# Kernel tuning notes

Hardware: AMD Instinct MI355X
Metric: run time of the kernel (lower is better)

The kernel has to match this reference:

```python
import jax, jax.numpy as jnp
import numpy as np

BS, N, C = 16, 128, 512
EPS = 1e-5


def setup_inputs() -> dict:
    key = jax.random.key(0)
    ks = jax.random.split(key, 6)
    x = jax.random.normal(ks[0], (BS, N, C), dtype=jnp.float32)
    y = jax.random.normal(ks[1], (BS, C), dtype=jnp.float32)
    # edge conv: Conv2d(2C -> 1, 1x1), init std sqrt(2/(1*1*1))
    conv_e_w = jax.random.normal(ks[2], (1, 2 * C), dtype=jnp.float32) * np.sqrt(2.0)
    conv_e_b = jnp.zeros((1,), dtype=jnp.float32)
    bn_e_g = jnp.ones((1,), dtype=jnp.float32)
    bn_e_b = jnp.zeros((1,), dtype=jnp.float32)
    bn_e_m = jnp.zeros((1,), dtype=jnp.float32)
    bn_e_v = jnp.ones((1,), dtype=jnp.float32)
    # feature conv: Conv2d(2C -> C, 1x1), init std sqrt(2/C)
    conv_f_w = jax.random.normal(ks[3], (C, 2 * C), dtype=jnp.float32) * np.sqrt(2.0 / C)
    conv_f_b = jnp.zeros((C,), dtype=jnp.float32)
    bn_f_g = jnp.ones((C,), dtype=jnp.float32)
    bn_f_b = jnp.zeros((C,), dtype=jnp.float32)
    bn_f_m = jnp.zeros((C,), dtype=jnp.float32)
    bn_f_v = jnp.ones((C,), dtype=jnp.float32)
    return {
        "x": x, "y": y,
        "conv_e_w": conv_e_w, "conv_e_b": conv_e_b,
        "bn_e_g": bn_e_g, "bn_e_b": bn_e_b, "bn_e_m": bn_e_m, "bn_e_v": bn_e_v,
        "conv_f_w": conv_f_w, "conv_f_b": conv_f_b,
        "bn_f_g": bn_f_g, "bn_f_b": bn_f_b, "bn_f_m": bn_f_m, "bn_f_v": bn_f_v,
    }


def reference(x, y, conv_e_w, conv_e_b, bn_e_g, bn_e_b, bn_e_m, bn_e_v,
              conv_f_w, conv_f_b, bn_f_g, bn_f_b, bn_f_m, bn_f_v):
    bs, n, c = x.shape
    # ---- Wcompute: pairwise |x_i - x_j| -> conv1x1(2C->1) + BN + mask + softmax ----
    diff = jnp.abs(x[:, :, None, :] - x[:, None, :, :])  # [bs, N, N, C]
    w_diff = conv_e_w[0, :c]   # weights on pairwise-diff channels
    w_y = conv_e_w[0, c:]      # weights on broadcast y channels
    # 1x1 conv collapses to einsum; y part is constant over (i, j)
    score = (jnp.einsum('bijc,c->bij', diff, w_diff)
             + (y @ w_y)[:, None, None] + conv_e_b[0])  # [bs, N, N]
    # BatchNorm2d(1), inference mode
    score = (score - bn_e_m[0]) * (bn_e_g[0] * jax.lax.rsqrt(bn_e_v[0] + EPS)) + bn_e_b[0]
    # mask diagonal (W_id * 1e8) then softmax over neighbors j
    score = score - jnp.eye(n, dtype=score.dtype)[None] * 1e8
    W = jax.nn.softmax(score, axis=2)  # [bs, N, N]
    # ---- Gconv: neighbor aggregation + conv1x1(2C->C) + BN + ReLU ----
    x_nb = jnp.einsum('bij,bjc->bic', W, x)       # [bs, N, C]
    h = jnp.concatenate([x, x_nb], axis=2)        # [bs, N, 2C]
    out = jnp.einsum('bnk,ck->bnc', h, conv_f_w) + conv_f_b  # [bs, N, C]
    # BatchNorm2d(C), inference mode (per-channel)
    out = (out - bn_f_m) * (bn_f_g * jax.lax.rsqrt(bn_f_v + EPS)) + bn_f_b
    return jax.nn.relu(out)
```

## Files before the change

kernel.cpp:

```cpp
#include <hip/hip_runtime.h>
#include <hip/hip_bf16.h>

#define NTOK 128
#define CHN  512
#define KTOT 1024
#define EPSV 1e-5f

typedef __attribute__((ext_vector_type(8))) short bf16x8;
typedef __attribute__((ext_vector_type(4))) float f32x4;

union BfPack4 { ushort4 u; __hip_bfloat16 h[4]; };


__global__ __launch_bounds__(256)
void k0_transpose(const float* __restrict__ xg,
                  float* __restrict__ xT,
                  __hip_bfloat16* __restrict__ xTbf,
                  __hip_bfloat16* __restrict__ hb,
                  const float* __restrict__ wf,
                  __hip_bfloat16* __restrict__ wfb)
{
    __shared__ float ts[64 * 68];
    const int t  = threadIdx.x;
    const int bk = blockIdx.x;
    const int b  = bk >> 4;
    const int jt = (bk >> 3) & 1;
    const int ct = bk & 7;
    const int j0 = jt * 64, c0 = ct * 64;

    const int jr = t >> 2, qd = t & 3;
    const float* src = xg + ((size_t)(b * NTOK) + j0 + jr) * CHN + c0 + qd * 16;
    float4 v0 = *(const float4*)&src[0];
    float4 v1 = *(const float4*)&src[4];
    float4 v2 = *(const float4*)&src[8];
    float4 v3 = *(const float4*)&src[12];
    *(float4*)&ts[jr * 68 + qd * 16 + 0]  = v0;
    *(float4*)&ts[jr * 68 + qd * 16 + 4]  = v1;
    *(float4*)&ts[jr * 68 + qd * 16 + 8]  = v2;
    *(float4*)&ts[jr * 68 + qd * 16 + 12] = v3;

    {
        __hip_bfloat16* hrow = hb + ((size_t)(b * NTOK) + j0 + jr) * KTOT + c0 + qd * 16;
        BfPack4 p;
        p.h[0]=__float2bfloat16(v0.x); p.h[1]=__float2bfloat16(v0.y);
        p.h[2]=__float2bfloat16(v0.z); p.h[3]=__float2bfloat16(v0.w);
        *(ushort4*)&hrow[0] = p.u;
        p.h[0]=__float2bfloat16(v1.x); p.h[1]=__float2bfloat16(v1.y);
        p.h[2]=__float2bfloat16(v1.z); p.h[3]=__float2bfloat16(v1.w);
        *(ushort4*)&hrow[4] = p.u;
        p.h[0]=__float2bfloat16(v2.x); p.h[1]=__float2bfloat16(v2.y);
        p.h[2]=__float2bfloat16(v2.z); p.h[3]=__float2bfloat16(v2.w);
        *(ushort4*)&hrow[8] = p.u;
        p.h[0]=__float2bfloat16(v3.x); p.h[1]=__float2bfloat16(v3.y);
        p.h[2]=__float2bfloat16(v3.z); p.h[3]=__float2bfloat16(v3.w);
        *(ushort4*)&hrow[12] = p.u;
    }

    {
        const int r   = 2 * bk + (t >> 7);
        const int col = (t & 127) * 8;
        const float* wsrc = wf + (size_t)r * KTOT + col;
        float4 u0 = *(const float4*)&wsrc[0];
        float4 u1 = *(const float4*)&wsrc[4];
        BfPack4 p;
        p.h[0]=__float2bfloat16(u0.x); p.h[1]=__float2bfloat16(u0.y);
        p.h[2]=__float2bfloat16(u0.z); p.h[3]=__float2bfloat16(u0.w);
        *(ushort4*)&wfb[(size_t)r * KTOT + col] = p.u;
        p.h[0]=__float2bfloat16(u1.x); p.h[1]=__float2bfloat16(u1.y);
        p.h[2]=__float2bfloat16(u1.z); p.h[3]=__float2bfloat16(u1.w);
        *(ushort4*)&wfb[(size_t)r * KTOT + col + 4] = p.u;
    }
    __syncthreads();

    const int cs = t >> 4, jj = (t & 15) * 4;
    #pragma unroll
    for (int m = 0; m < 4; ++m) {
        const int c = cs + 16 * m;
        float4 o;
        o.x = ts[(jj + 0) * 68 + c];
        o.y = ts[(jj + 1) * 68 + c];
        o.z = ts[(jj + 2) * 68 + c];
        o.w = ts[(jj + 3) * 68 + c];
        const size_t base = ((size_t)(b * CHN) + c0 + c) * NTOK + j0 + jj;
        *(float4*)&xT[base] = o;
        BfPack4 p;
        p.h[0]=__float2bfloat16(o.x); p.h[1]=__float2bfloat16(o.y);
        p.h[2]=__float2bfloat16(o.z); p.h[3]=__float2bfloat16(o.w);
        *(ushort4*)&xTbf[base] = p.u;
    }
}

__global__ __launch_bounds__(512)
void k1_fused(const float* __restrict__ xg,
              const float* __restrict__ xT,
              const float* __restrict__ wde,
              const float* __restrict__ bn_e_g,
              const float* __restrict__ bn_e_v,
              const __hip_bfloat16* __restrict__ xTbf,
              __hip_bfloat16* __restrict__ hb)
{
    __shared__ float        pLDS[4][8][128];
    __shared__ __hip_bfloat16 Wlds[16][136];

    const int t  = threadIdx.x;
    const int w  = t >> 6;
    const int l  = t & 63;
    const int bk = blockIdx.x;
    const int b  = bk >> 4;
    const int i0 = (bk & 15) * 8;

    {
        const int rp = __builtin_amdgcn_readfirstlane(w >> 2);
        const int cq = __builtin_amdgcn_readfirstlane(w & 3);
        const int c0 = cq * 128;
        const int r0 = rp * 4;

        const float* __restrict__ xtp = xT + ((size_t)(b * CHN) + c0) * NTOK + l;
        const float* __restrict__ xip = xg + ((size_t)(b * NTOK) + i0 + r0) * CHN + c0;
        const float* __restrict__ wdp = wde + c0;

        float a00=0.f,a01=0.f,a10=0.f,a11=0.f,a20=0.f,a21=0.f,a30=0.f,a31=0.f;
        #pragma unroll 8
        for (int c = 0; c < 128; ++c) {
            const float xj1 = xtp[c * NTOK];
            const float xj2 = xtp[c * NTOK + 64];
            const float wd  = wdp[c];
            const float xi0 = xip[0 * CHN + c];
            const float xi1 = xip[1 * CHN + c];
            const float xi2 = xip[2 * CHN + c];
            const float xi3 = xip[3 * CHN + c];
            a00 += fabsf(xi0 - xj1) * wd;  a01 += fabsf(xi0 - xj2) * wd;
            a10 += fabsf(xi1 - xj1) * wd;  a11 += fabsf(xi1 - xj2) * wd;
            a20 += fabsf(xi2 - xj1) * wd;  a21 += fabsf(xi2 - xj2) * wd;
            a30 += fabsf(xi3 - xj1) * wd;  a31 += fabsf(xi3 - xj2) * wd;
        }
        pLDS[cq][r0 + 0][l] = a00;  pLDS[cq][r0 + 0][l + 64] = a01;
        pLDS[cq][r0 + 1][l] = a10;  pLDS[cq][r0 + 1][l + 64] = a11;
        pLDS[cq][r0 + 2][l] = a20;  pLDS[cq][r0 + 2][l + 64] = a21;
        pLDS[cq][r0 + 3][l] = a30;  pLDS[cq][r0 + 3][l + 64] = a31;
    }
    __syncthreads();

    {
        float p1 = pLDS[0][w][l]      + pLDS[1][w][l]
                 + pLDS[2][w][l]      + pLDS[3][w][l];
        float p2 = pLDS[0][w][l + 64] + pLDS[1][w][l + 64]
                 + pLDS[2][w][l + 64] + pLDS[3][w][l + 64];
        const float sc = bn_e_g[0] * rsqrtf(bn_e_v[0] + EPSV);
        const int ir = i0 + w;
        float l1 = p1 * sc - (l == ir ? 1e8f : 0.f);
        float l2 = p2 * sc - (l + 64 == ir ? 1e8f : 0.f);

        float m = fmaxf(l1, l2);
        #pragma unroll
        for (int off = 32; off > 0; off >>= 1) m = fmaxf(m, __shfl_xor(m, off));
        const float e1 = __expf(l1 - m);
        const float e2 = __expf(l2 - m);
        float ssum = e1 + e2;
        #pragma unroll
        for (int off = 32; off > 0; off >>= 1) ssum += __shfl_xor(ssum, off);
        const float inv = 1.f / ssum;

        Wlds[w][l]          = __float2bfloat16(e1 * inv);
        Wlds[w][l + 64]     = __float2bfloat16(e2 * inv);
        Wlds[w + 8][l]      = __float2bfloat16(0.f);
        Wlds[w + 8][l + 64] = __float2bfloat16(0.f);
    }
    __syncthreads();

    {
        const int m16 = l & 15;
        const int q   = l >> 4;

        bf16x8 afr[4];
        #pragma unroll
        for (int kk = 0; kk < 4; ++kk)
            afr[kk] = *(const bf16x8*)&Wlds[m16][q * 8 + kk * 32];

        const int cbase = w * 64;
        #pragma unroll
        for (int ni = 0; ni < 4; ++ni) {
            const int c = cbase + ni * 16 + m16;
            const short* B0 = (const short*)xTbf + ((size_t)(b * CHN) + c) * NTOK + q * 8;
            f32x4 acc = {0.f, 0.f, 0.f, 0.f};
            #pragma unroll
            for (int kk = 0; kk < 4; ++kk) {
                const bf16x8 bfr = *(const bf16x8*)(B0 + kk * 32);
                acc = __builtin_amdgcn_mfma_f32_16x16x32_bf16(afr[kk], bfr, acc, 0, 0, 0);
            }
            if (q < 2) {
                #pragma unroll
                for (int r = 0; r < 4; ++r) {
                    const int i = i0 + q * 4 + r;
                    hb[(size_t)(b * NTOK + i) * KTOT + CHN + c] = __float2bfloat16(acc[r]);
                }
            }
        }
    }
}

__global__ __launch_bounds__(256)
void k2_gemm_bn_relu(const __hip_bfloat16* __restrict__ hbp,
                     const __hip_bfloat16* __restrict__ wfbp,
                     const float* __restrict__ fb,
                     const float* __restrict__ gg,
                     const float* __restrict__ bb,
                     const float* __restrict__ mm,
                     const float* __restrict__ vv,
                     float* __restrict__ out)
{
    const int blk  = blockIdx.x;
    const int r0   = (blk >> 3) << 6;
    const int c0   = (blk & 7) << 6;
    const int t    = threadIdx.x;
    const int w    = t >> 6;
    const int lane = t & 63;
    const int wm   = w & 1;
    const int wn   = w >> 1;
    const int m16  = lane & 15;
    const int qq   = lane >> 4;

    const short* A0 = (const short*)hbp  + (size_t)(r0 + wm * 32 + m16) * KTOT + qq * 8;
    const short* B0 = (const short*)wfbp + (size_t)(c0 + wn * 32 + m16) * KTOT + qq * 8;

    f32x4 acc00 = {0.f, 0.f, 0.f, 0.f};
    f32x4 acc01 = acc00, acc10 = acc00, acc11 = acc00;

    #pragma unroll 4
    for (int k0 = 0; k0 < KTOT; k0 += 32) {
        const bf16x8 aA = *(const bf16x8*)(A0 + k0);
        const bf16x8 aB = *(const bf16x8*)(A0 + 16 * KTOT + k0);
        const bf16x8 bA = *(const bf16x8*)(B0 + k0);
        const bf16x8 bB = *(const bf16x8*)(B0 + 16 * KTOT + k0);
        acc00 = __builtin_amdgcn_mfma_f32_16x16x32_bf16(aA, bA, acc00, 0, 0, 0);
        acc01 = __builtin_amdgcn_mfma_f32_16x16x32_bf16(aA, bB, acc01, 0, 0, 0);
        acc10 = __builtin_amdgcn_mfma_f32_16x16x32_bf16(aB, bA, acc10, 0, 0, 0);
        acc11 = __builtin_amdgcn_mfma_f32_16x16x32_bf16(aB, bB, acc11, 0, 0, 0);
    }

    #pragma unroll
    for (int ni = 0; ni < 2; ++ni) {
        const int c = c0 + wn * 32 + ni * 16 + m16;
        const float gf = gg[c] * rsqrtf(vv[c] + EPSV);
        const float ad = fb[c] - mm[c];
        const float bv = bb[c];
        const f32x4 acr0 = ni ? acc01 : acc00;
        const f32x4 acr1 = ni ? acc11 : acc10;
        #pragma unroll
        for (int r2 = 0; r2 < 4; ++r2) {
            int row = r0 + wm * 32 + qq * 4 + r2;
            float val = (acr0[r2] + ad) * gf + bv;
            out[(size_t)row * CHN + c] = fmaxf(val, 0.f);
            row += 16;
            val = (acr1[r2] + ad) * gf + bv;
            out[(size_t)row * CHN + c] = fmaxf(val, 0.f);
        }
    }
}

extern "C" void kernel_launch(void* const* d_in, const int* in_sizes, int n_in,
                              void* d_out, int out_size, void* d_ws, size_t ws_size,
                              hipStream_t stream) {
    const float* x        = (const float*)d_in[0];
    const float* conv_e_w = (const float*)d_in[2];
    const float* bn_e_g   = (const float*)d_in[4];
    const float* bn_e_v   = (const float*)d_in[7];
    const float* conv_f_w = (const float*)d_in[8];
    const float* conv_f_b = (const float*)d_in[9];
    const float* bn_f_g   = (const float*)d_in[10];
    const float* bn_f_b   = (const float*)d_in[11];
    const float* bn_f_m   = (const float*)d_in[12];
    const float* bn_f_v   = (const float*)d_in[13];
    float* out = (float*)d_out;

    char* ws = (char*)d_ws;
    float*           xT   = (float*)(ws);
    __hip_bfloat16*  hb   = (__hip_bfloat16*)(ws + (12u << 20));
    __hip_bfloat16*  wfb  = (__hip_bfloat16*)(ws + (16u << 20));
    __hip_bfloat16*  xTbf = (__hip_bfloat16*)(ws + (17u << 20) + (512u << 10));

    k0_transpose<<<256, 256, 0, stream>>>(x, xT, xTbf, hb, conv_f_w, wfb);
    k1_fused<<<256, 512, 0, stream>>>(x, xT, conv_e_w, bn_e_g, bn_e_v, xTbf, hb);
    k2_gemm_bn_relu<<<256, 256, 0, stream>>>(hb, wfb, conv_f_b, bn_f_g, bn_f_b,
                                             bn_f_m, bn_f_v, out);
}
```

Before: 120.4 us.

## Merge three kernels into one cooperative kernel with grid-wide syncs

Replaces the transpose, fused softmax/aggregation, and GEMM kernels with a single cooperative kernel of 256 blocks by 512 threads, separated by grid.sync barriers. This removes two kernel launch gaps and the drain between them. The pairwise-distance loop is also rewritten to process two channels at a time with float2 vectors and max(d,-d) for the absolute value. The trade-offs are grid-barrier cost, half the threads sitting idle in the GEMM phase, and higher LDS and register use limiting occupancy.

```diff
diff --git a/kernel.cpp b/kernel.cpp
--- a/kernel.cpp
+++ b/kernel.cpp
@@ -1,5 +1,8 @@
 #include <hip/hip_runtime.h>
 #include <hip/hip_bf16.h>
+#include <hip/hip_cooperative_groups.h>
+
+namespace cg = cooperative_groups;
 
 #define NTOK 128
 #define CHN  512
@@ -8,252 +11,241 @@
 
 typedef __attribute__((ext_vector_type(8))) short bf16x8;
 typedef __attribute__((ext_vector_type(4))) float f32x4;
+typedef __attribute__((ext_vector_type(2))) float f32x2;
 
 union BfPack4 { ushort4 u; __hip_bfloat16 h[4]; };
 
 
-__global__ __launch_bounds__(256)
-void k0_transpose(const float* __restrict__ xg,
-                  float* __restrict__ xT,
-                  __hip_bfloat16* __restrict__ xTbf,
-                  __hip_bfloat16* __restrict__ hb,
-                  const float* __restrict__ wf,
-                  __hip_bfloat16* __restrict__ wfb)
+__global__ __launch_bounds__(512)
+void mega(const float* __restrict__ xg,
+          float* __restrict__ xT,
+          __hip_bfloat16* __restrict__ xTbf,
+          __hip_bfloat16* __restrict__ hb,
+          const float* __restrict__ wf,
+          __hip_bfloat16* __restrict__ wfb,
+          const float* __restrict__ wde,
+          const float* __restrict__ bn_e_g,
+          const float* __restrict__ bn_e_v,
+          const float* __restrict__ fb,
+          const float* __restrict__ gg,
+          const float* __restrict__ bb,
+          const float* __restrict__ mm,
+          const float* __restrict__ vv,
+          float* __restrict__ out)
 {
-    __shared__ float ts[64 * 68];
-    const int t  = threadIdx.x;
-    const int bk = blockIdx.x;
-    const int b  = bk >> 4;
-    const int jt = (bk >> 3) & 1;
-    const int ct = bk & 7;
-    const int j0 = jt * 64, c0 = ct * 64;
-
-    const int jr = t >> 2, qd = t & 3;
-    const float* src = xg + ((size_t)(b * NTOK) + j0 + jr) * CHN + c0 + qd * 16;
-    float4 v0 = *(const float4*)&src[0];
-    float4 v1 = *(const float4*)&src[4];
-    float4 v2 = *(const float4*)&src[8];
-    float4 v3 = *(const float4*)&src[12];
-    *(float4*)&ts[jr * 68 + qd * 16 + 0]  = v0;
-    *(float4*)&ts[jr * 68 + qd * 16 + 4]  = v1;
-    *(float4*)&ts[jr * 68 + qd * 16 + 8]  = v2;
-    *(float4*)&ts[jr * 68 + qd * 16 + 12] = v3;
-
-    {
-        __hip_bfloat16* hrow = hb + ((size_t)(b * NTOK) + j0 + jr) * KTOT + c0 + qd * 16;
-        BfPack4 p;
-        p.h[0]=__float2bfloat16(v0.x); p.h[1]=__float2bfloat16(v0.y);
-        p.h[2]=__float2bfloat16(v0.z); p.h[3]=__float2bfloat16(v0.w);
-        *(ushort4*)&hrow[0] = p.u;
-        p.h[0]=__float2bfloat16(v1.x); p.h[1]=__float2bfloat16(v1.y);
-        p.h[2]=__float2bfloat16(v1.z); p.h[3]=__float2bfloat16(v1.w);
-        *(ushort4*)&hrow[4] = p.u;
-        p.h[0]=__float2bfloat16(v2.x); p.h[1]=__float2bfloat16(v2.y);
-        p.h[2]=__float2bfloat16(v2.z); p.h[3]=__float2bfloat16(v2.w);
-        *(ushort4*)&hrow[8] = p.u;
-        p.h[0]=__float2bfloat16(v3.x); p.h[1]=__float2bfloat16(v3.y);
-        p.h[2]=__float2bfloat16(v3.z); p.h[3]=__float2bfloat16(v3.w);
-        *(ushort4*)&hrow[12] = p.u;
-    }
-
-    {
-        const int r   = 2 * bk + (t >> 7);
-        const int col = (t & 127) * 8;
-        const float* wsrc = wf + (size_t)r * KTOT + col;
-        float4 u0 = *(const float4*)&wsrc[0];
-        float4 u1 = *(const float4*)&wsrc[4];
-        BfPack4 p;
-        p.h[0]=__float2bfloat16(u0.x); p.h[1]=__float2bfloat16(u0.y);
-        p.h[2]=__float2bfloat16(u0.z); p.h[3]=__float2bfloat16(u0.w);
-        *(ushort4*)&wfb[(size_t)r * KTOT + col] = p.u;
-        p.h[0]=__float2bfloat16(u1.x); p.h[1]=__float2bfloat16(u1.y);
-        p.h[2]=__float2bfloat16(u1.z); p.h[3]=__float2bfloat16(u1.w);
-        *(ushort4*)&wfb[(size_t)r * KTOT + col + 4] = p.u;
-    }
-    __syncthreads();
-
-    const int cs = t >> 4, jj = (t & 15) * 4;
-    #pragma unroll
-    for (int m = 0; m < 4; ++m) {
-        const int c = cs + 16 * m;
-        float4 o;
-        o.x = ts[(jj + 0) * 68 + c];
-        o.y = ts[(jj + 1) * 68 + c];
-        o.z = ts[(jj + 2) * 68 + c];
-        o.w = ts[(jj + 3) * 68 + c];
-        const size_t base = ((size_t)(b * CHN) + c0 + c) * NTOK + j0 + jj;
-        *(float4*)&xT[base] = o;
-        BfPack4 p;
-        p.h[0]=__float2bfloat16(o.x); p.h[1]=__float2bfloat16(o.y);
-        p.h[2]=__float2bfloat16(o.z); p.h[3]=__float2bfloat16(o.w);
-        *(ushort4*)&xTbf[base] = p.u;
-    }
-}
-
-__global__ __launch_bounds__(512)
-void k1_fused(const float* __restrict__ xg,
-              const float* __restrict__ xT,
-              const float* __restrict__ wde,
-              const float* __restrict__ bn_e_g,
-              const float* __restrict__ bn_e_v,
-              const __hip_bfloat16* __restrict__ xTbf,
-              __hip_bfloat16* __restrict__ hb)
-{
-    __shared__ float        pLDS[4][8][128];
+    __shared__ float          ts[64 * 68];
+    __shared__ float          pLDS[4][8][128];
     __shared__ __hip_bfloat16 Wlds[16][136];
+
+    cg::grid_group grid = cg::this_grid();
 
     const int t  = threadIdx.x;
     const int w  = t >> 6;
     const int l  = t & 63;
     const int bk = blockIdx.x;
-    const int b  = bk >> 4;
-    const int i0 = (bk & 15) * 8;
 
     {
-        const int rp = __builtin_amdgcn_readfirstlane(w >> 2);
-        const int cq = __builtin_amdgcn_readfirstlane(w & 3);
-        const int c0 = cq * 128;
-        const int r0 = rp * 4;
-
-        const float* __restrict__ xtp = xT + ((size_t)(b * CHN) + c0) * NTOK + l;
-        const float* __restrict__ xip = xg + ((size_t)(b * NTOK) + i0 + r0) * CHN + c0;
-        const float* __restrict__ wdp = wde + c0;
-
-        float a00=0.f,a01=0.f,a10=0.f,a11=0.f,a20=0.f,a21=0.f,a30=0.f,a31=0.f;
-        #pragma unroll 8
-        for (int c = 0; c < 128; ++c) {
-            const float xj1 = xtp[c * NTOK];
-            const float xj2 = xtp[c * NTOK + 64];
-            const float wd  = wdp[c];
-            const float xi0 = xip[0 * CHN + c];
-            const float xi1 = xip[1 * CHN + c];
-            const float xi2 = xip[2 * CHN + c];
-            const float xi3 = xip[3 * CHN + c];
-            a00 += fabsf(xi0 - xj1) * wd;  a01 += fabsf(xi0 - xj2) * wd;
-            a10 += fabsf(xi1 - xj1) * wd;  a11 += fabsf(xi1 - xj2) * wd;
-            a20 += fabsf(xi2 - xj1) * wd;  a21 += fabsf(xi2 - xj2) * wd;
-            a30 += fabsf(xi3 - xj1) * wd;  a31 += fabsf(xi3 - xj2) * wd;
-        }
-        pLDS[cq][r0 + 0][l] = a00;  pLDS[cq][r0 + 0][l + 64] = a01;
-        pLDS[cq][r0 + 1][l] = a10;  pLDS[cq][r0 + 1][l + 64] = a11;
-        pLDS[cq][r0 + 2][l] = a20;  pLDS[cq][r0 + 2][l + 64] = a21;
-        pLDS[cq][r0 + 3][l] = a30;  pLDS[cq][r0 + 3][l + 64] = a31;
+        const int b  = bk >> 4;
+        const int jt = (bk >> 3) & 1;
+        const int ct = bk & 7;
+        const int j0 = jt * 64, c0 = ct * 64;
+
+        const int jr = t >> 3, q8 = t & 7;
+        const float* src = xg + ((size_t)(b * NTOK) + j0 + jr) * CHN + c0 + q8 * 8;
+        float4 v0 = *(const float4*)&src[0];
+        float4 v1 = *(const float4*)&src[4];
+        *(float4*)&ts[jr * 68 + q8 * 8 + 0] = v0;
+        *(float4*)&ts[jr * 68 + q8 * 8 + 4] = v1;
+
+        {
+            __hip_bfloat16* hrow = hb + ((size_t)(b * NTOK) + j0 + jr) * KTOT + c0 + q8 * 8;
+            BfPack4 p;
+            p.h[0]=__float2bfloat16(v0.x); p.h[1]=__float2bfloat16(v0.y);
+            p.h[2]=__float2bfloat16(v0.z); p.h[3]=__float2bfloat16(v0.w);
+            *(ushort4*)&hrow[0] = p.u;
+            p.h[0]=__float2bfloat16(v1.x); p.h[1]=__float2bfloat16(v1.y);
+            p.h[2]=__float2bfloat16(v1.z); p.h[3]=__float2bfloat16(v1.w);
+            *(ushort4*)&hrow[4] = p.u;
+        }
+
+        {
+            const int r   = 2 * bk + (t >> 8);
+            const int col = (t & 255) * 4;
+            const float* wsrc = wf + (size_t)r * KTOT + col;
+            float4 u0 = *(const float4*)&wsrc[0];
+            BfPack4 p;
+            p.h[0]=__float2bfloat16(u0.x); p.h[1]=__float2bfloat16(u0.y);
+            p.h[2]=__float2bfloat16(u0.z); p.h[3]=__float2bfloat16(u0.w);
+            *(ushort4*)&wfb[(size_t)r * KTOT + col] = p.u;
+        }
+        __syncthreads();
+
+        const int c  = t >> 3;
+        const int jj = (t & 7) * 8;
+        float o[8];
+        #pragma unroll
+        for (int r = 0; r < 8; ++r) o[r] = ts[(jj + r) * 68 + c];
+        const size_t base = ((size_t)(b * CHN) + c0 + c) * NTOK + j0 + jj;
+        *(float4*)&xT[base + 0] = make_float4(o[0], o[1], o[2], o[3]);
+        *(float4*)&xT[base + 4] = make_float4(o[4], o[5], o[6], o[7]);
+        BfPack4 p;
+        p.h[0]=__float2bfloat16(o[0]); p.h[1]=__float2bfloat16(o[1]);
+        p.h[2]=__float2bfloat16(o[2]); p.h[3]=__float2bfloat16(o[3]);
+        *(ushort4*)&xTbf[base + 0] = p.u;
+        p.h[0]=__float2bfloat16(o[4]); p.h[1]=__float2bfloat16(o[5]);
+        p.h[2]=__float2bfloat16(o[6]); p.h[3]=__float2bfloat16(o[7]);
+        *(ushort4*)&xTbf[base + 4] = p.u;
     }
-    __syncthreads();
+
+    grid.sync();
 
     {
-        float p1 = pLDS[0][w][l]      + pLDS[1][w][l]
-                 + pLDS[2][w][l]      + pLDS[3][w][l];
-        float p2 = pLDS[0][w][l + 64] + pLDS[1][w][l + 64]
-                 + pLDS[2][w][l + 64] + pLDS[3][w][l + 64];
-        const float sc = bn_e_g[0] * rsqrtf(bn_e_v[0] + EPSV);
-        const int ir = i0 + w;
-        float l1 = p1 * sc - (l == ir ? 1e8f : 0.f);
-        float l2 = p2 * sc - (l + 64 == ir ? 1e8f : 0.f);
-
-        float m = fmaxf(l1, l2);
-        #pragma unroll
-        for (int off = 32; off > 0; off >>= 1) m = fmaxf(m, __shfl_xor(m, off));
-        const float e1 = __expf(l1 - m);
-        const float e2 = __expf(l2 - m);
-        float ssum = e1 + e2;
-        #pragma unroll
-        for (int off = 32; off > 0; off >>= 1) ssum += __shfl_xor(ssum, off);
-        const float inv = 1.f / ssum;
-
-        Wlds[w][l]          = __float2bfloat16(e1 * inv);
-        Wlds[w][l + 64]     = __float2bfloat16(e2 * inv);
-        Wlds[w + 8][l]      = __float2bfloat16(0.f);
-        Wlds[w + 8][l + 64] = __float2bfloat16(0.f);
-    }
-    __syncthreads();
-
-    {
-        const int m16 = l & 15;
-        const int q   = l >> 4;
-
-        bf16x8 afr[4];
-        #pragma unroll
-        for (int kk = 0; kk < 4; ++kk)
-            afr[kk] = *(const bf16x8*)&Wlds[m16][q * 8 + kk * 32];
-
-        const int cbase = w * 64;
-        #pragma unroll
-        for (int ni = 0; ni < 4; ++ni) {
-            const int c = cbase + ni * 16 + m16;
-            const short* B0 = (const short*)xTbf + ((size_t)(b * CHN) + c) * NTOK + q * 8;
-            f32x4 acc = {0.f, 0.f, 0.f, 0.f};
-            #pragma unroll
-            for (int kk = 0; kk < 4; ++kk) {
-                const bf16x8 bfr = *(const bf16x8*)(B0 + kk * 32);
-                acc = __builtin_amdgcn_mfma_f32_16x16x32_bf16(afr[kk], bfr, acc, 0, 0, 0);
+        const int b  = bk >> 4;
+        const int i0 = (bk & 15) * 8;
+
+        {
+            const int rp = __builtin_amdgcn_readfirstlane(w >> 2);
+            const int cq = __builtin_amdgcn_readfirstlane(w & 3);
+            const int c0 = cq * 128;
+            const int r0 = rp * 4;
+
+            const float* __restrict__ xtp = xT + ((size_t)(b * CHN) + c0) * NTOK + l;
+            const float* __restrict__ xip = xg + ((size_t)(b * NTOK) + i0 + r0) * CHN + c0;
+            const float* __restrict__ wdp = wde + c0;
+
+            f32x2 a00 = {0.f, 0.f};
+            f32x2 a01 = a00, a10 = a00, a11 = a00;
+            f32x2 a20 = a00, a21 = a00, a30 = a00, a31 = a00;
+
+            #pragma unroll 4
+            for (int cc = 0; cc < 128; cc += 2) {
+                const f32x2 xjA = { xtp[cc * NTOK],      xtp[(cc + 1) * NTOK] };
+                const f32x2 xjB = { xtp[cc * NTOK + 64], xtp[(cc + 1) * NTOK + 64] };
+                const f32x2 wd2 = *(const f32x2*)(wdp + cc);
+                const f32x2 xi0 = *(const f32x2*)(xip + 0 * CHN + cc);
+                const f32x2 xi1 = *(const f32x2*)(xip + 1 * CHN + cc);
+                const f32x2 xi2 = *(const f32x2*)(xip + 2 * CHN + cc);
+                const f32x2 xi3 = *(const f32x2*)(xip + 3 * CHN + cc);
+                f32x2 d;
+                d = xi0 - xjA; a00 += __builtin_elementwise_max(d, -d) * wd2;
+                d = xi0 - xjB; a01 += __builtin_elementwise_max(d, -d) * wd2;
+                d = xi1 - xjA; a10 += __builtin_elementwise_max(d, -d) * wd2;
+                d = xi1 - xjB; a11 += __builtin_elementwise_max(d, -d) * wd2;
+                d = xi2 - xjA; a20 += __builtin_elementwise_max(d, -d) * wd2;
+                d = xi2 - xjB; a21 += __builtin_elementwise_max(d, -d) * wd2;
+                d = xi3 - xjA; a30 += __builtin_elementwise_max(d, -d) * wd2;
+                d = xi3 - xjB; a31 += __builtin_elementwise_max(d, -d) * wd2;
             }
-            if (q < 2) {
+            pLDS[cq][r0 + 0][l] = a00.x + a00.y;  pLDS[cq][r0 + 0][l + 64] = a01.x + a01.y;
+            pLDS[cq][r0 + 1][l] = a10.x + a10.y;  pLDS[cq][r0 + 1][l + 64] = a11.x + a11.y;
+            pLDS[cq][r0 + 2][l] = a20.x + a20.y;  pLDS[cq][r0 + 2][l + 64] = a21.x + a21.y;
+            pLDS[cq][r0 + 3][l] = a30.x + a30.y;  pLDS[cq][r0 + 3][l + 64] = a31.x + a31.y;
+        }
+        __syncthreads();
+
+        {
+            float p1 = pLDS[0][w][l]      + pLDS[1][w][l]
+                     + pLDS[2][w][l]      + pLDS[3][w][l];
+            float p2 = pLDS[0][w][l + 64] + pLDS[1][w][l + 64]
+                     + pLDS[2][w][l + 64] + pLDS[3][w][l + 64];
+            const float sc = bn_e_g[0] * rsqrtf(bn_e_v[0] + EPSV);
+            const int ir = i0 + w;
+            float l1 = p1 * sc - (l == ir ? 1e8f : 0.f);
+            float l2 = p2 * sc - (l + 64 == ir ? 1e8f : 0.f);
+
+            float m = fmaxf(l1, l2);
+            #pragma unroll
+            for (int off = 32; off > 0; off >>= 1) m = fmaxf(m, __shfl_xor(m, off));
+            const float e1 = __expf(l1 - m);
+            const float e2 = __expf(l2 - m);
+            float ssum = e1 + e2;
+            #pragma unroll
+            for (int off = 32; off > 0; off >>= 1) ssum += __shfl_xor(ssum, off);
+            const float inv = 1.f / ssum;
+
+            Wlds[w][l]          = __float2bfloat16(e1 * inv);
+            Wlds[w][l + 64]     = __float2bfloat16(e2 * inv);
+            Wlds[w + 8][l]      = __float2bfloat16(0.f);
+            Wlds[w + 8][l + 64] = __float2bfloat16(0.f);
+        }
+        __syncthreads();
+
+        {
+            const int m16 = l & 15;
+            const int q   = l >> 4;
+
+            bf16x8 afr[4];
+            #pragma unroll
+            for (int kk = 0; kk < 4; ++kk)
+                afr[kk] = *(const bf16x8*)&Wlds[m16][q * 8 + kk * 32];
+
+            const int cbase = w * 64;
+            #pragma unroll
+            for (int ni = 0; ni < 4; ++ni) {
+                const int c = cbase + ni * 16 + m16;
+                const short* B0 = (const short*)xTbf + ((size_t)(b * CHN) + c) * NTOK + q * 8;
+                f32x4 acc = {0.f, 0.f, 0.f, 0.f};
                 #pragma unroll
-                for (int r = 0; r < 4; ++r) {
-                    const int i = i0 + q * 4 + r;
-                    hb[(size_t)(b * NTOK + i) * KTOT + CHN + c] = __float2bfloat16(acc[r]);
+                for (int kk = 0; kk < 4; ++kk) {
+                    const bf16x8 bfr = *(const bf16x8*)(B0 + kk * 32);
+                    acc = __builtin_amdgcn_mfma_f32_16x16x32_bf16(afr[kk], bfr, acc, 0, 0, 0);
+                }
+                if (q < 2) {
+                    #pragma unroll
+                    for (int r = 0; r < 4; ++r) {
+                        const int i = i0 + q * 4 + r;
+                        hb[(size_t)(b * NTOK + i) * KTOT + CHN + c] = __float2bfloat16(acc[r]);
+                    }
                 }
             }
         }
     }
-}
-
-__global__ __launch_bounds__(256)
-void k2_gemm_bn_relu(const __hip_bfloat16* __restrict__ hbp,
-                     const __hip_bfloat16* __restrict__ wfbp,
-                     const float* __restrict__ fb,
-                     const float* __restrict__ gg,
-                     const float* __restrict__ bb,
-                     const float* __restrict__ mm,
-                     const float* __restrict__ vv,
-                     float* __restrict__ out)
-{
-    const int blk  = blockIdx.x;
-    const int r0   = (blk >> 3) << 6;
-    const int c0   = (blk & 7) << 6;
-    const int t    = threadIdx.x;
-    const int w    = t >> 6;
-    const int lane = t & 63;
-    const int wm   = w & 1;
-    const int wn   = w >> 1;
-    const int m16  = lane & 15;
-    const int qq   = lane >> 4;
-
-    const short* A0 = (const short*)hbp  + (size_t)(r0 + wm * 32 + m16) * KTOT + qq * 8;
-    const short* B0 = (const short*)wfbp + (size_t)(c0 + wn * 32 + m16) * KTOT + qq * 8;
-
-    f32x4 acc00 = {0.f, 0.f, 0.f, 0.f};
-    f32x4 acc01 = acc00, acc10 = acc00, acc11 = acc00;
-
-    #pragma unroll 4
-    for (int k0 = 0; k0 < KTOT; k0 += 32) {
-        const bf16x8 aA = *(const bf16x8*)(A0 + k0);
-        const bf16x8 aB = *(const bf16x8*)(A0 + 16 * KTOT + k0);
-        const bf16x8 bA = *(const bf16x8*)(B0 + k0);
-        const bf16x8 bB = *(const bf16x8*)(B0 + 16 * KTOT + k0);
-        acc00 = __builtin_amdgcn_mfma_f32_16x16x32_bf16(aA, bA, acc00, 0, 0, 0);
-        acc01 = __builtin_amdgcn_mfma_f32_16x16x32_bf16(aA, bB, acc01, 0, 0, 0);
-        acc10 = __builtin_amdgcn_mfma_f32_16x16x32_bf16(aB, bA, acc10, 0, 0, 0);
-        acc11 = __builtin_amdgcn_mfma_f32_16x16x32_bf16(aB, bB, acc11, 0, 0, 0);
-    }
-
-    #pragma unroll
-    for (int ni = 0; ni < 2; ++ni) {
-        const int c = c0 + wn * 32 + ni * 16 + m16;
-        const float gf = gg[c] * rsqrtf(vv[c] + EPSV);
-        const float ad = fb[c] - mm[c];
-        const float bv = bb[c];
-        const f32x4 acr0 = ni ? acc01 : acc00;
-        const f32x4 acr1 = ni ? acc11 : acc10;
+
+    grid.sync();
+
+    if (t < 256) {
+        const int r0   = (bk >> 3) << 6;
+        const int c0   = (bk & 7) << 6;
+        const int wm   = w & 1;
+        const int wn   = w >> 1;
+        const int m16  = l & 15;
+        const int qq   = l >> 4;
+
+        const short* A0 = (const short*)hb  + (size_t)(r0 + wm * 32 + m16) * KTOT + qq * 8;
+        const short* B0 = (const short*)wfb + (size_t)(c0 + wn * 32 + m16) * KTOT + qq * 8;
+
+        f32x4 acc00 = {0.f, 0.f, 0.f, 0.f};
+        f32x4 acc01 = acc00, acc10 = acc00, acc11 = acc00;
+
+        #pragma unroll 4
+        for (int k0 = 0; k0 < KTOT; k0 += 32) {
+            const bf16x8 aA = *(const bf16x8*)(A0 + k0);
+            const bf16x8 aB = *(const bf16x8*)(A0 + 16 * KTOT + k0);
+            const bf16x8 bA = *(const bf16x8*)(B0 + k0);
+            const bf16x8 bB = *(const bf16x8*)(B0 + 16 * KTOT + k0);
+            acc00 = __builtin_amdgcn_mfma_f32_16x16x32_bf16(aA, bA, acc00, 0, 0, 0);
+            acc01 = __builtin_amdgcn_mfma_f32_16x16x32_bf16(aA, bB, acc01, 0, 0, 0);
+            acc10 = __builtin_amdgcn_mfma_f32_16x16x32_bf16(aB, bA, acc10, 0, 0, 0);
+            acc11 = __builtin_amdgcn_mfma_f32_16x16x32_bf16(aB, bB, acc11, 0, 0, 0);
+        }
+
         #pragma unroll
-        for (int r2 = 0; r2 < 4; ++r2) {
-            int row = r0 + wm * 32 + qq * 4 + r2;
-            float val = (acr0[r2] + ad) * gf + bv;
-            out[(size_t)row * CHN + c] = fmaxf(val, 0.f);
-            row += 16;
-            val = (acr1[r2] + ad) * gf + bv;
-            out[(size_t)row * CHN + c] = fmaxf(val, 0.f);
+        for (int ni = 0; ni < 2; ++ni) {
+            const int c = c0 + wn * 32 + ni * 16 + m16;
+            const float gf = gg[c] * rsqrtf(vv[c] + EPSV);
+            const float ad = fb[c] - mm[c];
+            const float bv = bb[c];
+            const f32x4 acr0 = ni ? acc01 : acc00;
+            const f32x4 acr1 = ni ? acc11 : acc10;
+            #pragma unroll
+            for (int r2 = 0; r2 < 4; ++r2) {
+                int row = r0 + wm * 32 + qq * 4 + r2;
+                float val = (acr0[r2] + ad) * gf + bv;
+                out[(size_t)row * CHN + c] = fmaxf(val, 0.f);
+                row += 16;
+                val = (acr1[r2] + ad) * gf + bv;
+                out[(size_t)row * CHN + c] = fmaxf(val, 0.f);
+            }
         }
     }
 }
@@ -279,8 +271,13 @@
     __hip_bfloat16*  wfb  = (__hip_bfloat16*)(ws + (16u << 20));
     __hip_bfloat16*  xTbf = (__hip_bfloat16*)(ws + (17u << 20) + (512u << 10));
 
-    k0_transpose<<<256, 256, 0, stream>>>(x, xT, xTbf, hb, conv_f_w, wfb);
-    k1_fused<<<256, 512, 0, stream>>>(x, xT, conv_e_w, bn_e_g, bn_e_v, xTbf, hb);
-    k2_gemm_bn_relu<<<256, 256, 0, stream>>>(hb, wfb, conv_f_b, bn_f_g, bn_f_b,
-                                             bn_f_m, bn_f_v, out);
+    void* args[] = {
+        (void*)&x, (void*)&xT, (void*)&xTbf, (void*)&hb,
+        (void*)&conv_f_w, (void*)&wfb, (void*)&conv_e_w,
+        (void*)&bn_e_g, (void*)&bn_e_v,
+        (void*)&conv_f_b, (void*)&bn_f_g, (void*)&bn_f_b,
+        (void*)&bn_f_m, (void*)&bn_f_v, (void*)&out
+    };
+    hipLaunchCooperativeKernel((const void*)mega, dim3(256), dim3(512),
+                               args, 0, stream);
 }
```

Result: slower. 200.4 us (+66.5%).
